# Kernel optimization log

Measured on AMD Instinct MI355X. Metric: run time of the kernel, lower is better.

Reference implementation:

```python
import jax, jax.numpy as jnp
import numpy as np

N = 1024
H = 128


def setup_inputs() -> dict:
    key = jax.random.key(0)
    k1, k2, k3, k4, k5, k6 = jax.random.split(key, 6)
    s = 1.0 / np.sqrt(H)
    return {
        "node_feats": jax.random.normal(k1, (N, H), dtype=jnp.float32),
        "edge_attr": jax.random.normal(k2, (N * N, H), dtype=jnp.float32),
        "We": jax.random.uniform(k3, (H, H), jnp.float32, -s, s),
        "be": jax.random.uniform(k4, (H,), jnp.float32, -s, s),
        "Wi": jax.random.uniform(k5, (H, H), jnp.float32, -s, s),
        "Wj": jax.random.uniform(k6, (H, H), jnp.float32, -s, s),
    }


def reference(node_feats, edge_attr, We, be, Wi, Wj):
    # f_ij: [N^2, H] linear with bias
    f_ij = edge_attr @ We.T + be
    # f_i, f_j: [N, H] linears without bias
    f_i = node_feats @ Wi.T
    f_j = node_feats @ Wj.T
    # torch.matmul on 1-D vectors -> scalar dot; broadcast into each H-wide row.
    dots = jnp.einsum("ih,jh->ij", f_i, f_j)  # [N, N]
    fi_fj = dots.reshape(-1, 1)                 # [N^2, 1], broadcasts over H
    return jax.nn.relu(f_ij + fi_fj)
```

## Files before the change

### kernel.cpp

```cpp
#include <hip/hip_runtime.h>
#include <hip/hip_bf16.h>
#include <stdint.h>
#include <stddef.h>

typedef __bf16 bf16_t;
typedef __bf16 bf16x8 __attribute__((ext_vector_type(8)));
typedef float  f32x4  __attribute__((ext_vector_type(4)));
typedef float  f32x16 __attribute__((ext_vector_type(16)));

#define NN 1024
#define H  128
#define GRID 2048

__global__ void k_cvt_we(const float* __restrict__ src, bf16_t* __restrict__ dst) {
    int i = blockIdx.x * 256 + threadIdx.x;
    if (i < H * H) dst[i] = (bf16_t)src[i];
}

__global__ void k_proj(const float* __restrict__ node,
                       const float* __restrict__ Wi,
                       const float* __restrict__ Wj,
                       bf16_t* __restrict__ fi,
                       bf16_t* __restrict__ fj) {
    __shared__ float nrow[H];
    const int row = blockIdx.x;
    const int t   = threadIdx.x;
    const int h   = t & (H - 1);
    const int sel = t >> 7;
    if (t < H) nrow[t] = node[(size_t)row * H + t];
    __syncthreads();
    const float* w = (sel ? Wj : Wi) + (size_t)h * H;
    float acc = 0.f;
    #pragma unroll
    for (int k4 = 0; k4 < H / 4; ++k4) {
        f32x4 wv = *(const f32x4*)(w + k4 * 4);
        f32x4 nv = *(const f32x4*)(&nrow[k4 * 4]);
        acc += nv[0] * wv[0] + nv[1] * wv[1] + nv[2] * wv[2] + nv[3] * wv[3];
    }
    bf16_t* dst = sel ? fj : fi;
    dst[(size_t)row * H + h] = (bf16_t)acc;
}

__global__ __launch_bounds__(256, 4)
void k_dots(const bf16_t* __restrict__ fi,
            const bf16_t* __restrict__ fj,
            float* __restrict__ dots) {
    const int t    = threadIdx.x;
    const int wave = t >> 6;
    const int lane = t & 63;
    const int l15  = lane & 15;
    const int g    = lane >> 4;

    const int bm    = blockIdx.x >> 3;
    const int bn    = blockIdx.x & 7;
    const int ibase = bm * 64 + wave * 16;
    const int jbase = bn * 128;

    f32x4 acc[8];
    #pragma unroll
    for (int nt = 0; nt < 8; ++nt) acc[nt] = (f32x4){0.f, 0.f, 0.f, 0.f};

    const bf16_t* a = fi + (size_t)(ibase + l15) * H + g * 8;

    #pragma unroll
    for (int kst = 0; kst < 4; ++kst) {
        bf16x8 af = *(const bf16x8*)(a + kst * 32);
        #pragma unroll
        for (int nt = 0; nt < 8; ++nt) {
            bf16x8 bf = *(const bf16x8*)(fj + (size_t)(jbase + nt * 16 + l15) * H + kst * 32 + g * 8);
            acc[nt] = __builtin_amdgcn_mfma_f32_16x16x32_bf16(af, bf, acc[nt], 0, 0, 0);
        }
    }

    const int rbase = ibase + g * 4;
    #pragma unroll
    for (int r = 0; r < 4; ++r)
        #pragma unroll
        for (int nt = 0; nt < 8; ++nt)
            dots[(size_t)(rbase + r) * NN + jbase + nt * 16 + l15] = acc[nt][r];
}

__device__ __forceinline__ void gl_lds16(const float* g, float* l) {
    __builtin_amdgcn_global_load_lds(
        (const __attribute__((address_space(1))) unsigned int*)g,
        (__attribute__((address_space(3))) unsigned int*)l,
        16, 0, 0);
}

__global__ __launch_bounds__(256)
void k_main(const float* __restrict__ edge,
            const bf16_t* __restrict__ web,
            const float* __restrict__ be,
            const float* __restrict__ dots,
            float* __restrict__ out) {
    __shared__ __align__(16) float bufA[64][H];
    __shared__ __align__(16) float bufB[64][H];
    __shared__ float ldots[512];

    const int t    = threadIdx.x;
    const int w    = t >> 6;
    const int lane = t & 63;
    const int l31  = lane & 31;
    const int h    = lane >> 5;
    const int wm   = w & 1;
    const int wn   = w >> 1;
    const size_t base = (size_t)blockIdx.x * 512;

    ldots[t]       = dots[base + t];
    ldots[256 + t] = dots[base + 256 + t];

    bf16x8 wfr[2][8];
    {
        const bf16_t* wp = web + (size_t)(wn * 64 + l31) * H + h * 8;
        #pragma unroll
        for (int nt = 0; nt < 2; ++nt)
            #pragma unroll
            for (int kk = 0; kk < 8; ++kk)
                wfr[nt][kk] = *(const bf16x8*)(wp + (size_t)(nt * 32) * H + kk * 16);
    }
    float bias[2];
    #pragma unroll
    for (int nt = 0; nt < 2; ++nt) bias[nt] = be[wn * 64 + nt * 32 + l31];

    #define STAGE(K, BUFP)                                                       \
        {                                                                        \
            const char* tb = (const char*)(edge + (base + (size_t)(K) * 64) * H); \
            _Pragma("unroll")                                                    \
            for (int i = 0; i < 8; ++i) {                                        \
                const int rr = w * 16 + 2 * i + h;                               \
                gl_lds16((const float*)(tb + rr * 512 + ((l31 * 16) ^ ((rr & 7) << 4))), \
                         &BUFP[w * 16 + 2 * i][0]);                              \
            }                                                                    \
        }

    STAGE(0, bufA)

    const int sw = (l31 & 7) << 4;

    #pragma unroll 1
    for (int k = 0; k < 8; ++k) {
        __syncthreads();

        const char* crow = (const char*)((k & 1) ? &bufB[0][0] : &bufA[0][0])
                         + (wm * 32 + l31) * 512;

        f32x4 ua[8], ub[8];
        #pragma unroll
        for (int kk = 0; kk < 8; ++kk) {
            ua[kk] = *(const f32x4*)(crow + ((kk * 64 + h * 32 +  0) ^ sw));
            ub[kk] = *(const f32x4*)(crow + ((kk * 64 + h * 32 + 16) ^ sw));
        }

        if (k < 7) {
            if (k & 1) { STAGE(k + 1, bufA) }
            else       { STAGE(k + 1, bufB) }
        }

        f32x4 dv[4];
        #pragma unroll
        for (int b = 0; b < 4; ++b)
            dv[b] = *(const f32x4*)(&ldots[k * 64 + wm * 32 + 4 * h + 8 * b]);

        f32x16 acc[2];
        #pragma unroll
        for (int nt = 0; nt < 2; ++nt)
            #pragma unroll
            for (int r = 0; r < 16; ++r)
                acc[nt][r] = bias[nt] + dv[r >> 2][r & 3];

        #pragma unroll
        for (int kk = 0; kk < 8; ++kk) {
            bf16x8 af;
            #pragma unroll
            for (int e = 0; e < 4; ++e) {
                af[e]     = (bf16_t)ua[kk][e];
                af[e + 4] = (bf16_t)ub[kk][e];
            }
            #pragma unroll
            for (int nt = 0; nt < 2; ++nt)
                acc[nt] = __builtin_amdgcn_mfma_f32_32x32x16_bf16(af, wfr[nt][kk], acc[nt], 0, 0, 0);
        }

        float* orow = out + (base + (size_t)k * 64 + wm * 32 + 4 * h) * H + wn * 64 + l31;
        #pragma unroll
        for (int nt = 0; nt < 2; ++nt)
            #pragma unroll
            for (int r = 0; r < 16; ++r)
                orow[((r & 3) + 8 * (r >> 2)) * H + nt * 32] = fmaxf(acc[nt][r], 0.f);
    }
    #undef STAGE
}

extern "C" void kernel_launch(void* const* d_in, const int* in_sizes, int n_in,
                              void* d_out, int out_size, void* d_ws, size_t ws_size,
                              hipStream_t stream) {
    const float* node = (const float*)d_in[0];
    const float* edge = (const float*)d_in[1];
    const float* We   = (const float*)d_in[2];
    const float* be   = (const float*)d_in[3];
    const float* Wi   = (const float*)d_in[4];
    const float* Wj   = (const float*)d_in[5];
    float* out = (float*)d_out;

    char* w = (char*)d_ws;
    bf16_t* fi_bf = (bf16_t*)w;
    bf16_t* fj_bf = (bf16_t*)(w + (256 << 10));
    float*  dots  = (float*)(w + (512 << 10));
    bf16_t* web   = (bf16_t*)(w + (512 << 10) + (4 << 20));

    k_cvt_we<<<(H * H + 255) / 256, 256, 0, stream>>>(We, web);
    k_proj<<<NN, 256, 0, stream>>>(node, Wi, Wj, fi_bf, fj_bf);
    k_dots<<<128, 256, 0, stream>>>(fi_bf, fj_bf, dots);
    k_main<<<GRID, 256, 0, stream>>>(edge, web, be, dots, out);
}
```

Baseline: 237.3 us.

## Stage edge tiles through registers instead of direct global-to-LDS loads; fuse We conversion

The main kernel now prefetches the next edge tile into registers with ordinary vector loads and writes it into shared memory after the current tile's compute and stores. This replaces the async global_load_lds path, making the prefetch an explicit register-staged software pipeline at the cost of more VGPRs and extra LDS write instructions. The standalone We-to-bf16 conversion kernel is folded into the projection kernel, removing one launch.

Result: no change. 238.1 us (+0.3%).

```diff
diff --git a/kernel.cpp b/kernel.cpp
--- a/kernel.cpp
+++ b/kernel.cpp
@@ -12,21 +12,24 @@
 #define H  128
 #define GRID 2048
 
-__global__ void k_cvt_we(const float* __restrict__ src, bf16_t* __restrict__ dst) {
-    int i = blockIdx.x * 256 + threadIdx.x;
-    if (i < H * H) dst[i] = (bf16_t)src[i];
-}
-
 __global__ void k_proj(const float* __restrict__ node,
                        const float* __restrict__ Wi,
                        const float* __restrict__ Wj,
+                       const float* __restrict__ We,
                        bf16_t* __restrict__ fi,
-                       bf16_t* __restrict__ fj) {
+                       bf16_t* __restrict__ fj,
+                       bf16_t* __restrict__ web) {
     __shared__ float nrow[H];
     const int row = blockIdx.x;
     const int t   = threadIdx.x;
     const int h   = t & (H - 1);
     const int sel = t >> 7;
+
+    if (blockIdx.x < 64) {
+        const int i = blockIdx.x * 256 + t;
+        web[i] = (bf16_t)We[i];
+    }
+
     if (t < H) nrow[t] = node[(size_t)row * H + t];
     __syncthreads();
     const float* w = (sel ? Wj : Wi) + (size_t)h * H;
@@ -80,13 +83,6 @@
             dots[(size_t)(rbase + r) * NN + jbase + nt * 16 + l15] = acc[nt][r];
 }
 
-__device__ __forceinline__ void gl_lds16(const float* g, float* l) {
-    __builtin_amdgcn_global_load_lds(
-        (const __attribute__((address_space(1))) unsigned int*)g,
-        (__attribute__((address_space(3))) unsigned int*)l,
-        16, 0, 0);
-}
-
 __global__ __launch_bounds__(256)
 void k_main(const float* __restrict__ edge,
             const bf16_t* __restrict__ web,
@@ -122,18 +118,27 @@
     #pragma unroll
     for (int nt = 0; nt < 2; ++nt) bias[nt] = be[wn * 64 + nt * 32 + l31];
 
-    #define STAGE(K, BUFP)                                                       \
+    #define LOADT(K, V)                                                          \
         {                                                                        \
             const char* tb = (const char*)(edge + (base + (size_t)(K) * 64) * H); \
             _Pragma("unroll")                                                    \
             for (int i = 0; i < 8; ++i) {                                        \
                 const int rr = w * 16 + 2 * i + h;                               \
-                gl_lds16((const float*)(tb + rr * 512 + ((l31 * 16) ^ ((rr & 7) << 4))), \
-                         &BUFP[w * 16 + 2 * i][0]);                              \
+                V[i] = *(const f32x4*)(tb + rr * 512 + ((l31 * 16) ^ ((rr & 7) << 4))); \
             }                                                                    \
         }
-
-    STAGE(0, bufA)
+    #define WRITET(BUFP, V)                                                      \
+        {                                                                        \
+            _Pragma("unroll")                                                    \
+            for (int i = 0; i < 8; ++i)                                          \
+                *(f32x4*)((char*)&BUFP[w * 16 + 2 * i][0] + h * 512 + l31 * 16) = V[i]; \
+        }
+
+    {
+        f32x4 v0[8];
+        LOADT(0, v0)
+        WRITET(bufA, v0)
+    }
 
     const int sw = (l31 & 7) << 4;
 
@@ -141,19 +146,16 @@
     for (int k = 0; k < 8; ++k) {
         __syncthreads();
 
+        f32x4 vn[8];
+        if (k < 7) LOADT(k + 1, vn)
+
         const char* crow = (const char*)((k & 1) ? &bufB[0][0] : &bufA[0][0])
                          + (wm * 32 + l31) * 512;
-
         f32x4 ua[8], ub[8];
         #pragma unroll
         for (int kk = 0; kk < 8; ++kk) {
             ua[kk] = *(const f32x4*)(crow + ((kk * 64 + h * 32 +  0) ^ sw));
             ub[kk] = *(const f32x4*)(crow + ((kk * 64 + h * 32 + 16) ^ sw));
-        }
-
-        if (k < 7) {
-            if (k & 1) { STAGE(k + 1, bufA) }
-            else       { STAGE(k + 1, bufB) }
         }
 
         f32x4 dv[4];
@@ -187,8 +189,14 @@
             #pragma unroll
             for (int r = 0; r < 16; ++r)
                 orow[((r & 3) + 8 * (r >> 2)) * H + nt * 32] = fmaxf(acc[nt][r], 0.f);
-    }
-    #undef STAGE
+
+        if (k < 7) {
+            if (k & 1) { WRITET(bufA, vn) }
+            else       { WRITET(bufB, vn) }
+        }
+    }
+    #undef LOADT
+    #undef WRITET
 }
 
 extern "C" void kernel_launch(void* const* d_in, const int* in_sizes, int n_in,
@@ -208,8 +216,7 @@
     float*  dots  = (float*)(w + (512 << 10));
     bf16_t* web   = (bf16_t*)(w + (512 << 10) + (4 << 20));
 
-    k_cvt_we<<<(H * H + 255) / 256, 256, 0, stream>>>(We, web);
-    k_proj<<<NN, 256, 0, stream>>>(node, Wi, Wj, fi_bf, fj_bf);
+    k_proj<<<NN, 256, 0, stream>>>(node, Wi, Wj, We, fi_bf, fj_bf, web);
     k_dots<<<128, 256, 0, stream>>>(fi_bf, fj_bf, dots);
     k_main<<<GRID, 256, 0, stream>>>(edge, web, be, dots, out);
 }
```
